# Kernel optimization log

Hardware: AMD Instinct MI355X
Metric: run time of the kernel (lower is better)

Reference implementation:

```python
import jax, jax.numpy as jnp
import numpy as np

N = 64       # number of sites / qubits
CHI = 32     # bond dimension chi_max
D = 2        # physical dim (== label dim l)
BATCH = 262144
STD = 0.001  # init noise, matches MPS.initialize_params


def setup_inputs() -> dict:
    key = jax.random.key(0)
    kx, k0, kc, kn = jax.random.split(key, 4)
    # X: [N, batch, d] -- each X[i] contracts with site i's physical leg
    X = jax.random.normal(kx, (N, BATCH, D), dtype=jnp.float32)
    # core0: (d, chi), one-hot column 0 plus noise
    core0 = jnp.zeros((D, CHI), jnp.float32).at[:, 0].set(1.0)
    core0 = core0 + STD * jax.random.normal(k0, (D, CHI), dtype=jnp.float32)
    # middle cores: (N-1, chi, d, chi), identity stacked over d plus noise
    eye = jnp.eye(CHI, dtype=jnp.float32)                      # (chi, chi)
    mid = jnp.broadcast_to(eye[:, None, :], (CHI, D, CHI))     # (chi, d, chi)
    cores = jnp.broadcast_to(mid, (N - 1, CHI, D, CHI))
    cores = cores + STD * jax.random.normal(kc, (N - 1, CHI, D, CHI), dtype=jnp.float32)
    # coreN: (chi, d), one-hot row 0 plus noise
    coreN = jnp.zeros((CHI, D), jnp.float32).at[0].set(1.0)
    coreN = coreN + STD * jax.random.normal(kn, (CHI, D), dtype=jnp.float32)
    return {"X": X, "core0": core0, "cores": cores, "coreN": coreN}


def reference(X, core0, cores, coreN):
    # Sequential MPS chain contraction:
    #   v <- X[0] @ core0                       (batch, chi)
    #   v <- einsum('ab,bqc,aq->ac', v, core_i, X[i])   for i = 1..N-1
    #   out = |v @ coreN|                       (batch, l)
    v0 = jnp.einsum('aq,qc->ac', X[0], core0)  # (B, chi)

    def step(v, inp):
        x, core = inp  # x: (B, d), core: (chi, d, chi)
        # contract bond then physical leg, keeping only (B, chi) resident
        v_new = jnp.einsum('ab,bqc,aq->ac', v, core, x)
        return v_new, None

    v, _ = jax.lax.scan(step, v0, (X[1:], cores))
    out = jnp.einsum('ac,cq->aq', v, coreN)    # (B, l)
    return jnp.abs(out)
```

## Files before the change

kernel.cpp:

```cpp
#include <hip/hip_runtime.h>
#include <hip/hip_bf16.h>

#define BATCH 262144
#define NSITES 64
#define NJ 4
#define BLOCK_BATCH 256

typedef __attribute__((ext_vector_type(8))) short short8;
typedef __attribute__((ext_vector_type(4))) float f32x4;

__device__ __forceinline__ unsigned cvt_pk_bf16(float a, float b) {
  unsigned r;
  asm("v_cvt_pk_bf16_f32 %0, %1, %2" : "=v"(r) : "v"(a), "v"(b));
  return r;
}

__device__ __forceinline__ int qmap(int k) {
  return (((k >> 2) & 1) << 4) | (((k >> 3) & 3) << 2) | (k & 3);
}

__global__ void pack_E(const float* __restrict__ cores, unsigned short* __restrict__ Ep) {
  int idx = blockIdx.x * 256 + threadIdx.x;
  if (idx >= (NSITES - 1) * 2048) return;
  int t = idx & 7;
  int l = (idx >> 3) & 63;
  int f = (idx >> 9) & 3;
  int p = idx >> 11;
  int g = l >> 4, col = l & 15;
  int m = f >> 1, h = f & 1;
  int k = 8 * g + t, c = h * 16 + col;
  int b = qmap(k);
  float val = cores[((p * 32 + b) * 2 + m) * 32 + c] - ((b == c) ? 1.0f : 0.0f);
  __hip_bfloat16 hv = __float2bfloat16(val);
  Ep[idx] = *(unsigned short*)&hv;
}

__device__ __forceinline__ void gll16(const void* g, void* l) {
  __builtin_amdgcn_global_load_lds(
      (const __attribute__((address_space(1))) unsigned*)g,
      (__attribute__((address_space(3))) unsigned*)l, 16, 0, 0);
}

#define BODYJ(jj, xx0, xx1)                                                     \
  {                                                                             \
    union { short8 s8; unsigned u[4]; } vb;                                     \
    vb.u[0] = cvt_pk_bf16(v[jj][0], v[jj][1]);                                  \
    vb.u[1] = cvt_pk_bf16(v[jj][2], v[jj][3]);                                  \
    vb.u[2] = cvt_pk_bf16(v[jj][4], v[jj][5]);                                  \
    vb.u[3] = cvt_pk_bf16(v[jj][6], v[jj][7]);                                  \
    const f32x4 z = {0.f, 0.f, 0.f, 0.f};                                       \
    f32x4 r0lo = __builtin_amdgcn_mfma_f32_16x16x32_bf16(A0, vb.s8, z, 0, 0, 0); \
    f32x4 r0hi = __builtin_amdgcn_mfma_f32_16x16x32_bf16(A1, vb.s8, z, 0, 0, 0); \
    f32x4 r1lo = __builtin_amdgcn_mfma_f32_16x16x32_bf16(A2, vb.s8, z, 0, 0, 0); \
    f32x4 r1hi = __builtin_amdgcn_mfma_f32_16x16x32_bf16(A3, vb.s8, z, 0, 0, 0); \
    const float ss = (xx0) + (xx1);                                             \
    _Pragma("unroll") for (int t = 0; t < 4; ++t) {                             \
      v[jj][t] = ss * v[jj][t] + (xx0)*r0lo[t] + (xx1)*r1lo[t];                 \
      v[jj][4 + t] = ss * v[jj][4 + t] + (xx0)*r0hi[t] + (xx1)*r1hi[t];         \
    }                                                                           \
  }

__global__ __launch_bounds__(256, 4) void mps_chain_kernel(
    const float* __restrict__ X, const float* __restrict__ core0,
    const float* __restrict__ coreN, const unsigned short* __restrict__ Ep,
    float* __restrict__ out) {
  __shared__ __align__(16) char Elds[4][4096];
  __shared__ __align__(16) char Xlds[4][2048];
  const int tid = threadIdx.x;
  const int lane = tid & 63;
  const int wave = tid >> 6;
  const int col = lane & 15;
  const int g = lane >> 4;
  const int abase = blockIdx.x * BLOCK_BATCH + wave * (16 * NJ);
  const char* Epc = (const char*)Ep;
  const char* Xc = (const char*)X;
  const size_t xblock = (size_t)blockIdx.x * (BLOCK_BATCH * 8);

  float c0[2][8];
#pragma unroll
  for (int m = 0; m < 2; ++m)
#pragma unroll
    for (int t = 0; t < 8; ++t) c0[m][t] = core0[m * 32 + qmap(8 * g + t)];

  float v[NJ][8];
#pragma unroll
  for (int jj = 0; jj < NJ; ++jj) {
    const float2 xj =
        *(const float2*)(X + 2 * (size_t)(abase + jj * 16 + col));
#pragma unroll
    for (int t = 0; t < 8; ++t) v[jj][t] = xj.x * c0[0][t] + xj.y * c0[1][t];
  }

#pragma unroll
  for (int k = 1; k <= 3; ++k) {
    gll16(Epc + (size_t)(k - 1) * 4096 + (size_t)tid * 16,
          &Elds[k][wave * 1024]);
    if (lane < 32)
      gll16(Xc + (size_t)k * (BATCH * 8) + xblock + wave * 512 + lane * 16,
            &Xlds[k][wave * 512]);
  }
  asm volatile("s_waitcnt vmcnt(4)" ::: "memory");
  __builtin_amdgcn_s_barrier();

#pragma unroll 1
  for (int s = 1; s < NSITES; ++s) {
    const int rs = s & 3;
    const int ws = (s + 3) & 3;
    const int pk = (s + 3 < NSITES) ? s + 3 : NSITES - 1;
    gll16(Epc + (size_t)(pk - 1) * 4096 + (size_t)tid * 16,
          &Elds[ws][wave * 1024]);
    if (lane < 32)
      gll16(Xc + (size_t)pk * (BATCH * 8) + xblock + wave * 512 + lane * 16,
            &Xlds[ws][wave * 512]);
    asm volatile("s_waitcnt vmcnt(4)" ::: "memory");

    const short8* ep = (const short8*)&Elds[rs][lane * 16];
    const short8 A0 = ep[0], A1 = ep[64], A2 = ep[128], A3 = ep[192];
    const float* xp = (const float*)&Xlds[rs][wave * 512 + col * 8];
    const float x00 = xp[0],  x01 = xp[1];
    const float x10 = xp[32], x11 = xp[33];
    const float x20 = xp[64], x21 = xp[65];
    const float x30 = xp[96], x31 = xp[97];

    BODYJ(0, x00, x01);
    BODYJ(1, x10, x11);
    BODYJ(2, x20, x21);
    BODYJ(3, x30, x31);

    __builtin_amdgcn_s_barrier();
  }

  float cN[8][2];
#pragma unroll
  for (int t = 0; t < 8; ++t) {
    cN[t][0] = coreN[qmap(8 * g + t) * 2 + 0];
    cN[t][1] = coreN[qmap(8 * g + t) * 2 + 1];
  }
#pragma unroll
  for (int jj = 0; jj < NJ; ++jj) {
    float p0 = 0.f, p1 = 0.f;
#pragma unroll
    for (int t = 0; t < 8; ++t) {
      p0 += v[jj][t] * cN[t][0];
      p1 += v[jj][t] * cN[t][1];
    }
    p0 += __shfl_xor(p0, 16);
    p0 += __shfl_xor(p0, 32);
    p1 += __shfl_xor(p1, 16);
    p1 += __shfl_xor(p1, 32);
    if (g == 0) {
      const int a = abase + jj * 16 + col;
      out[2 * a] = fabsf(p0);
      out[2 * a + 1] = fabsf(p1);
    }
  }
}

extern "C" void kernel_launch(void* const* d_in, const int* in_sizes, int n_in,
                              void* d_out, int out_size, void* d_ws, size_t ws_size,
                              hipStream_t stream) {
  const float* X = (const float*)d_in[0];
  const float* core0 = (const float*)d_in[1];
  const float* cores = (const float*)d_in[2];
  const float* coreN = (const float*)d_in[3];
  float* out = (float*)d_out;
  unsigned short* Ep = (unsigned short*)d_ws;

  hipLaunchKernelGGL(pack_E, dim3(((NSITES - 1) * 2048 + 255) / 256), dim3(256), 0, stream,
                     cores, Ep);
  hipLaunchKernelGGL(mps_chain_kernel, dim3(BATCH / BLOCK_BATCH), dim3(256), 0, stream, X,
                     core0, coreN, Ep, out);
}
```

Before: 103.0 us.

## Double per-wave batch tile and use packed float2 math for state update

Doubles the batch rows each wave handles (NJ 4→8, block batch 256→512), so each loaded core tile in LDS and each barrier covers twice the MFMA work, and all threads now take part in the X prefetch. The per-row state update is rewritten on float2 vectors so the compiler can emit packed FMA instructions. In exchange, register use per thread roughly doubles while launch bounds still ask for 4 blocks per CU, which risks spills or lower occupancy, and the grid is halved.

```diff
diff --git a/kernel.cpp b/kernel.cpp
--- a/kernel.cpp
+++ b/kernel.cpp
@@ -3,17 +3,20 @@
 
 #define BATCH 262144
 #define NSITES 64
-#define NJ 4
-#define BLOCK_BATCH 256
+#define NJ 8
+#define BLOCK_BATCH 512
 
 typedef __attribute__((ext_vector_type(8))) short short8;
 typedef __attribute__((ext_vector_type(4))) float f32x4;
+typedef __attribute__((ext_vector_type(2))) float f32x2;
 
 __device__ __forceinline__ unsigned cvt_pk_bf16(float a, float b) {
   unsigned r;
   asm("v_cvt_pk_bf16_f32 %0, %1, %2" : "=v"(r) : "v"(a), "v"(b));
   return r;
 }
+#define LOH2(r) (__builtin_shufflevector((r), (r), 0, 1))
+#define HIH2(r) (__builtin_shufflevector((r), (r), 2, 3))
 
 __device__ __forceinline__ int qmap(int k) {
   return (((k >> 2) & 1) << 4) | (((k >> 3) & 3) << 2) | (k & 3);
@@ -44,20 +47,21 @@
 #define BODYJ(jj, xx0, xx1)                                                     \
   {                                                                             \
     union { short8 s8; unsigned u[4]; } vb;                                     \
-    vb.u[0] = cvt_pk_bf16(v[jj][0], v[jj][1]);                                  \
-    vb.u[1] = cvt_pk_bf16(v[jj][2], v[jj][3]);                                  \
-    vb.u[2] = cvt_pk_bf16(v[jj][4], v[jj][5]);                                  \
-    vb.u[3] = cvt_pk_bf16(v[jj][6], v[jj][7]);                                  \
+    vb.u[0] = cvt_pk_bf16(w2[jj][0][0], w2[jj][0][1]);                          \
+    vb.u[1] = cvt_pk_bf16(w2[jj][1][0], w2[jj][1][1]);                          \
+    vb.u[2] = cvt_pk_bf16(w2[jj][2][0], w2[jj][2][1]);                          \
+    vb.u[3] = cvt_pk_bf16(w2[jj][3][0], w2[jj][3][1]);                          \
     const f32x4 z = {0.f, 0.f, 0.f, 0.f};                                       \
     f32x4 r0lo = __builtin_amdgcn_mfma_f32_16x16x32_bf16(A0, vb.s8, z, 0, 0, 0); \
     f32x4 r0hi = __builtin_amdgcn_mfma_f32_16x16x32_bf16(A1, vb.s8, z, 0, 0, 0); \
     f32x4 r1lo = __builtin_amdgcn_mfma_f32_16x16x32_bf16(A2, vb.s8, z, 0, 0, 0); \
     f32x4 r1hi = __builtin_amdgcn_mfma_f32_16x16x32_bf16(A3, vb.s8, z, 0, 0, 0); \
     const float ss = (xx0) + (xx1);                                             \
-    _Pragma("unroll") for (int t = 0; t < 4; ++t) {                             \
-      v[jj][t] = ss * v[jj][t] + (xx0)*r0lo[t] + (xx1)*r1lo[t];                 \
-      v[jj][4 + t] = ss * v[jj][4 + t] + (xx0)*r0hi[t] + (xx1)*r1hi[t];         \
-    }                                                                           \
+    const f32x2 sv = {ss, ss}, x0v = {(xx0), (xx0)}, x1v = {(xx1), (xx1)};      \
+    w2[jj][0] = sv * w2[jj][0] + x0v * LOH2(r0lo) + x1v * LOH2(r1lo);           \
+    w2[jj][1] = sv * w2[jj][1] + x0v * HIH2(r0lo) + x1v * HIH2(r1lo);           \
+    w2[jj][2] = sv * w2[jj][2] + x0v * LOH2(r0hi) + x1v * LOH2(r1hi);           \
+    w2[jj][3] = sv * w2[jj][3] + x0v * HIH2(r0hi) + x1v * HIH2(r1hi);           \
   }
 
 __global__ __launch_bounds__(256, 4) void mps_chain_kernel(
@@ -65,7 +69,7 @@
     const float* __restrict__ coreN, const unsigned short* __restrict__ Ep,
     float* __restrict__ out) {
   __shared__ __align__(16) char Elds[4][4096];
-  __shared__ __align__(16) char Xlds[4][2048];
+  __shared__ __align__(16) char Xlds[4][4096];
   const int tid = threadIdx.x;
   const int lane = tid & 63;
   const int wave = tid >> 6;
@@ -82,22 +86,23 @@
 #pragma unroll
     for (int t = 0; t < 8; ++t) c0[m][t] = core0[m * 32 + qmap(8 * g + t)];
 
-  float v[NJ][8];
+  f32x2 w2[NJ][4];
 #pragma unroll
   for (int jj = 0; jj < NJ; ++jj) {
-    const float2 xj =
-        *(const float2*)(X + 2 * (size_t)(abase + jj * 16 + col));
+    const float2 xj = *(const float2*)(X + 2 * (size_t)(abase + jj * 16 + col));
 #pragma unroll
-    for (int t = 0; t < 8; ++t) v[jj][t] = xj.x * c0[0][t] + xj.y * c0[1][t];
+    for (int q = 0; q < 4; ++q) {
+      w2[jj][q][0] = xj.x * c0[0][2 * q] + xj.y * c0[1][2 * q];
+      w2[jj][q][1] = xj.x * c0[0][2 * q + 1] + xj.y * c0[1][2 * q + 1];
+    }
   }
 
 #pragma unroll
   for (int k = 1; k <= 3; ++k) {
     gll16(Epc + (size_t)(k - 1) * 4096 + (size_t)tid * 16,
           &Elds[k][wave * 1024]);
-    if (lane < 32)
-      gll16(Xc + (size_t)k * (BATCH * 8) + xblock + wave * 512 + lane * 16,
-            &Xlds[k][wave * 512]);
+    gll16(Xc + (size_t)k * (BATCH * 8) + xblock + (size_t)tid * 16,
+          &Xlds[k][wave * 1024]);
   }
   asm volatile("s_waitcnt vmcnt(4)" ::: "memory");
   __builtin_amdgcn_s_barrier();
@@ -109,23 +114,28 @@
     const int pk = (s + 3 < NSITES) ? s + 3 : NSITES - 1;
     gll16(Epc + (size_t)(pk - 1) * 4096 + (size_t)tid * 16,
           &Elds[ws][wave * 1024]);
-    if (lane < 32)
-      gll16(Xc + (size_t)pk * (BATCH * 8) + xblock + wave * 512 + lane * 16,
-            &Xlds[ws][wave * 512]);
+    gll16(Xc + (size_t)pk * (BATCH * 8) + xblock + (size_t)tid * 16,
+          &Xlds[ws][wave * 1024]);
     asm volatile("s_waitcnt vmcnt(4)" ::: "memory");
 
     const short8* ep = (const short8*)&Elds[rs][lane * 16];
     const short8 A0 = ep[0], A1 = ep[64], A2 = ep[128], A3 = ep[192];
-    const float* xp = (const float*)&Xlds[rs][wave * 512 + col * 8];
-    const float x00 = xp[0],  x01 = xp[1];
-    const float x10 = xp[32], x11 = xp[33];
-    const float x20 = xp[64], x21 = xp[65];
-    const float x30 = xp[96], x31 = xp[97];
+    const float* xp = (const float*)&Xlds[rs][wave * 1024 + col * 8];
+    float xv0[NJ], xv1[NJ];
+#pragma unroll
+    for (int jj = 0; jj < NJ; ++jj) {
+      xv0[jj] = xp[jj * 32];
+      xv1[jj] = xp[jj * 32 + 1];
+    }
 
-    BODYJ(0, x00, x01);
-    BODYJ(1, x10, x11);
-    BODYJ(2, x20, x21);
-    BODYJ(3, x30, x31);
+    BODYJ(0, xv0[0], xv1[0]);
+    BODYJ(1, xv0[1], xv1[1]);
+    BODYJ(2, xv0[2], xv1[2]);
+    BODYJ(3, xv0[3], xv1[3]);
+    BODYJ(4, xv0[4], xv1[4]);
+    BODYJ(5, xv0[5], xv1[5]);
+    BODYJ(6, xv0[6], xv1[6]);
+    BODYJ(7, xv0[7], xv1[7]);
 
     __builtin_amdgcn_s_barrier();
   }
@@ -141,8 +151,8 @@
     float p0 = 0.f, p1 = 0.f;
 #pragma unroll
     for (int t = 0; t < 8; ++t) {
-      p0 += v[jj][t] * cN[t][0];
-      p1 += v[jj][t] * cN[t][1];
+      p0 += w2[jj][t >> 1][t & 1] * cN[t][0];
+      p1 += w2[jj][t >> 1][t & 1] * cN[t][1];
     }
     p0 += __shfl_xor(p0, 16);
     p0 += __shfl_xor(p0, 32);
```

Result: no change. 103.5 us (+0.6%).
